# Kernel tuning notes

Measured on AMD Instinct MI355X. Metric: run time of the kernel, lower is better.

Reference implementation:

```python
import jax, jax.numpy as jnp
import numpy as np

V = 50257      # num_class
H = 512        # hid_size
EMB = 256      # embedding_size
E = 128        # emb_cond_size
COND_RANGE = (10, 20, 30)
NCSEQ = 100    # num_cond_seq_class
T, B = 64, 32
TC = 32        # cond_seq length


def _gru_scan(x, h0, Wih, Whh, bih, bhh):
    """PyTorch-convention GRU. x: [T,B,in], h0: [B,Hd]. Gate order: r,z,n."""
    Hd = h0.shape[-1]
    xw = jnp.einsum('tbi,gi->tbg', x, Wih) + bih  # [T,B,3H]

    def step(h, xw_t):
        hw = h @ Whh.T + bhh
        r = jax.nn.sigmoid(xw_t[:, :Hd] + hw[:, :Hd])
        z = jax.nn.sigmoid(xw_t[:, Hd:2 * Hd] + hw[:, Hd:2 * Hd])
        n = jnp.tanh(xw_t[:, 2 * Hd:] + r * hw[:, 2 * Hd:])
        hn = (1.0 - z) * n + z * h
        return hn, hn

    hT, outs = jax.lax.scan(step, h0, xw)
    return outs, hT


def setup_inputs() -> dict:
    key = jax.random.key(0)
    ks = jax.random.split(key, 24)
    s = 0.02
    inp = {
        'input_data': jax.random.randint(ks[0], (T, B), 0, V),
        'condition': jnp.stack([jax.random.randint(ks[1 + i], (B,), 0, COND_RANGE[i]) for i in range(3)], 0),
        'cond_seq': jax.random.randint(ks[4], (TC, B), 0, NCSEQ),
        'emb_cond_0': jax.random.normal(ks[5], (COND_RANGE[0], E)) * s,
        'emb_cond_1': jax.random.normal(ks[6], (COND_RANGE[1], E)) * s,
        'emb_cond_2': jax.random.normal(ks[7], (COND_RANGE[2], E)) * s,
        'cond_seq_emb': jax.random.normal(ks[8], (NCSEQ, E)) * s,
        'embedding': jax.random.normal(ks[9], (V, EMB)) * s,
        'attn_W': jax.random.normal(ks[10], (H, E + H)) * s,
        'attn_b': jnp.zeros((H,), jnp.float32),
        'v_W': jax.random.normal(ks[11], (1, H)) * s,
        'gru_Wih': jax.random.normal(ks[12], (3 * H, EMB)) * s,
        'gru_Whh': jax.random.normal(ks[13], (3 * H, H)) * s,
        'gru_bih': jnp.zeros((3 * H,), jnp.float32),
        'gru_bhh': jnp.zeros((3 * H,), jnp.float32),
        'cgru_Wih': jax.random.normal(ks[14], (3 * E, E)) * s,
        'cgru_Whh': jax.random.normal(ks[15], (3 * E, E)) * s,
        'cgru_bih': jnp.zeros((3 * E,), jnp.float32),
        'cgru_bhh': jnp.zeros((3 * E,), jnp.float32),
        'dense_W': jax.random.normal(ks[16], (V, E + EMB + H)) * s,
        'dense_b': jnp.zeros((V,), jnp.float32),
    }
    return inp


def reference(input_data, condition, cond_seq,
              emb_cond_0, emb_cond_1, emb_cond_2, cond_seq_emb, embedding,
              attn_W, attn_b, v_W,
              gru_Wih, gru_Whh, gru_bih, gru_bhh,
              cgru_Wih, cgru_Whh, cgru_bih, cgru_bhh,
              dense_W, dense_b):
    Tl, Bl = input_data.shape
    # conditional embeddings: [num_cond, B, E]
    tables = (emb_cond_0, emb_cond_1, emb_cond_2)
    cond_emb = jnp.stack([tables[i][condition[i]] for i in range(3)], axis=0)
    # conditional sequence GRU encoder: [TC, B, E]
    cseq_in = cond_seq_emb[cond_seq]
    cseq_out, _ = _gru_scan(cseq_in, jnp.zeros((Bl, E), cseq_in.dtype),
                            cgru_Wih, cgru_Whh, cgru_bih, cgru_bhh)
    enc = jnp.concatenate([cond_emb, cseq_out], axis=0)  # [S, B, E]
    enc_b = jnp.transpose(enc, (1, 0, 2))                # [B, S, E]

    # Bahdanau attention: split attn weight into encoder/decoder parts
    W_e = attn_W[:, :E]   # [H, E]
    W_h = attn_W[:, E:]   # [H, H]
    enc_proj = jnp.einsum('bse,he->bsh', enc_b, W_e)     # precompute once

    x_emb = embedding[input_data]                        # [T, B, EMB]
    xw = jnp.einsum('tbi,gi->tbg', x_emb, gru_Wih) + gru_bih  # [T, B, 3H]

    def step(h, inputs):
        xe_t, xw_t = inputs
        # attention against previous hidden h
        score = jnp.tanh(enc_proj + (h @ W_h.T + attn_b)[:, None, :]) @ v_W[0]  # [B,S]
        w = jax.nn.softmax(score, axis=1)
        c = jnp.einsum('bs,bse->be', w, enc_b)           # [B, E]
        # GRU cell
        hw = h @ gru_Whh.T + gru_bhh
        r = jax.nn.sigmoid(xw_t[:, :H] + hw[:, :H])
        z = jax.nn.sigmoid(xw_t[:, H:2 * H] + hw[:, H:2 * H])
        n = jnp.tanh(xw_t[:, 2 * H:] + r * hw[:, 2 * H:])
        hn = (1.0 - z) * n + z * h
        # output head uses context, input embedding and PREVIOUS hidden h
        logits = jnp.concatenate([c, xe_t, h], axis=-1) @ dense_W.T + dense_b
        pred = jax.nn.log_softmax(logits, axis=-1)
        return hn, (pred, w)

    h0 = jnp.zeros((Bl, H), x_emb.dtype)
    hT, (total_pred, weights) = jax.lax.scan(step, h0, (x_emb, xw))
    return total_pred, hT[None, :, :], weights


if __name__ == '__main__':
    out = reference(**setup_inputs())
    print([o.shape for o in out])
```

## Files before the change

### kernel.cpp

```cpp
#include <hip/hip_runtime.h>
#include <hip/hip_bf16.h>
#include <hip/hip_cooperative_groups.h>
#include <math.h>

namespace cg = cooperative_groups;

#define Tt 64
#define Bb 32
#define Hh 512
#define EMBe 256
#define Ee 128
#define Ss 35
#define Vv 50257
#define Kk 896
#define TCc 32
#define VPAD 50304
#define NTILE 393

typedef __bf16 bf16_t;
typedef __bf16 bf16x4 __attribute__((ext_vector_type(4)));
typedef __bf16 bf16x8 __attribute__((ext_vector_type(8)));
typedef float f32x4 __attribute__((ext_vector_type(4)));

#define POIS32 0x7FC07FC0u

__device__ __forceinline__ float sigf(float x){ return 1.f/(1.f + expf(-x)); }

__device__ __forceinline__ void gll16(const void* g, void* l){
  __builtin_amdgcn_global_load_lds(
      (const __attribute__((address_space(1))) unsigned int*)g,
      (__attribute__((address_space(3))) unsigned int*)l, 16, 0, 0);
}

#define DOT4(acc, W_, H_) acc += (W_).x*(H_).x + (W_).y*(H_).y + (W_).z*(H_).z + (W_).w*(H_).w

__global__ void k_cond_emb(const int* __restrict__ cond, const float* __restrict__ t0,
                           const float* __restrict__ t1, const float* __restrict__ t2,
                           float* __restrict__ enc){
  int g = blockIdx.x*blockDim.x + threadIdx.x;
  if (g >= 3*Bb*Ee) return;
  int i = g/(Bb*Ee); int b = (g/Ee)%Bb; int e = g%Ee;
  const float* tbl = (i==0)? t0 : (i==1)? t1 : t2;
  int ci = cond[i*Bb + b];
  enc[(size_t)i*Bb*Ee + b*Ee + e] = tbl[(size_t)ci*Ee + e];
}

__global__ void k_cxw(const int* __restrict__ cond_seq, const float* __restrict__ cemb,
                      const float* __restrict__ Wih, const float* __restrict__ bih,
                      float* __restrict__ cxw){
  __shared__ float es[Ee];
  int row = blockIdx.x; int tid = threadIdx.x;
  int idx = cond_seq[row];
  es[tid] = cemb[(size_t)idx*Ee + tid];
  __syncthreads();
  const float4* hp = (const float4*)es;
  for (int q = 0; q < 3; ++q){
    int g = q*Ee + tid;
    const float4* wr = (const float4*)(Wih + (size_t)g*Ee);
    float acc = bih[g];
    #pragma unroll 8
    for (int k = 0; k < Ee/4; ++k){ float4 w4 = wr[k]; float4 h4 = hp[k]; DOT4(acc, w4, h4); }
    cxw[(size_t)row*(3*Ee) + g] = acc;
  }
}

__global__ void k_xemb(const int* __restrict__ input_data, const float* __restrict__ emb,
                       bf16_t* __restrict__ xe){
  int row = blockIdx.x, tid = threadIdx.x;
  int idx = input_data[row];
  xe[(size_t)row*EMBe + tid] = (bf16_t)emb[(size_t)idx*EMBe + tid];
}

__global__ void k_ctrans(const float* __restrict__ W, float* __restrict__ WT){
  int idx = blockIdx.x*256 + threadIdx.x;
  if (idx >= 3*Ee*Ee) return;
  int g = idx/Ee, k = idx%Ee;
  WT[(size_t)k*(3*Ee) + g] = W[idx];
}

__global__ void k_cseq_scan(const float* __restrict__ cxw, const float* __restrict__ WT,
                            const float* __restrict__ bhh, float* __restrict__ enc){
  __shared__ float hs[Ee];
  int b = blockIdx.x; int j = threadIdx.x;
  hs[j] = 0.f; __syncthreads();
  float b0 = bhh[j], b1 = bhh[Ee+j], b2 = bhh[2*Ee+j];
  for (int t = 0; t < TCc; ++t){
    const float* xp = cxw + ((size_t)t*Bb + b)*(3*Ee);
    float a0=b0, a1=b1, a2=b2;
    #pragma unroll 4
    for (int k = 0; k < Ee; ++k){
      float hk = hs[k];
      const float* wr = WT + (size_t)k*(3*Ee);
      a0 += hk * wr[j];
      a1 += hk * wr[Ee + j];
      a2 += hk * wr[2*Ee + j];
    }
    float r = sigf(xp[j] + a0);
    float z = sigf(xp[Ee + j] + a1);
    float n = tanhf(xp[2*Ee + j] + r*a2);
    float hcur = hs[j];
    float hn = (1.f - z)*n + z*hcur;
    __syncthreads();
    hs[j] = hn;
    enc[(size_t)(3+t)*Bb*Ee + b*Ee + j] = hn;
    __syncthreads();
  }
}

__global__ void k_encproj(const float* __restrict__ enc, const float* __restrict__ attn_W,
                          float* __restrict__ enc_proj){
  __shared__ float es[Ee];
  int blk = blockIdx.x; int tid = threadIdx.x;
  int b = blk/Ss, s = blk%Ss;
  if (tid < Ee) es[tid] = enc[(size_t)s*Bb*Ee + b*Ee + tid];
  __syncthreads();
  const float4* hp = (const float4*)es;
  for (int q = 0; q < 2; ++q){
    int hh = q*256 + tid;
    const float4* wr = (const float4*)(attn_W + (size_t)hh*(Ee+Hh));
    float acc = 0.f;
    #pragma unroll 8
    for (int k = 0; k < Ee/4; ++k){ float4 w4 = wr[k]; float4 h4 = hp[k]; DOT4(acc, w4, h4); }
    enc_proj[(size_t)blk*Hh + hh] = acc;
  }
}

#define HSLOT (Bb*Hh)

__global__ void k_poison(bf16_t* __restrict__ hsteps){
  size_t i = (size_t)blockIdx.x*256 + threadIdx.x;
  size_t total = (size_t)(Tt+1)*HSLOT/2;
  if (i >= total) return;
  unsigned v = (i < HSLOT/2) ? 0u : POIS32;
  __hip_atomic_store((unsigned*)hsteps + i, v, __ATOMIC_RELAXED, __HIP_MEMORY_SCOPE_AGENT);
}

#define SCAN_BLOCKS_L 128
#define SCAN_WORK 16
#define SCAN_THREADS 384
#define WSL_STRIDE 520
#define HST_STRIDE 520
#define GW_STRIDE 104
#define SCAN_LDS (96*WSL_STRIDE*2 + Bb*HST_STRIDE*2 + Bb*GW_STRIDE*4)
#define NCH 11

__global__ __launch_bounds__(SCAN_THREADS) void k_scan_coop(
    const float* __restrict__ xw, const float* __restrict__ Whh,
    const float* __restrict__ bhh, float* __restrict__ h_all,
    bf16_t* __restrict__ hsteps, const float* __restrict__ Wd,
    bf16_t* __restrict__ Wb, int wbf){
  extern __shared__ char smem[];
  const int tid = threadIdx.x;
  const int blk = blockIdx.x;

  if (blk >= SCAN_WORK){
    if (wbf){
      size_t total = (size_t)VPAD*Kk/8;
      size_t stride = (size_t)(SCAN_BLOCKS_L - SCAN_WORK)*SCAN_THREADS;
      for (size_t c = (size_t)(blk - SCAN_WORK)*SCAN_THREADS + tid; c < total; c += stride){
        size_t i = c*8;
        size_t row = i / Kk;
        int col = (int)(i % Kk);
        bf16x8 o;
        if (row < Vv){
          float4 f0 = *(const float4*)(Wd + i);
          float4 f1 = *(const float4*)(Wd + i + 4);
          o[0]=(bf16_t)f0.x; o[1]=(bf16_t)f0.y; o[2]=(bf16_t)f0.z; o[3]=(bf16_t)f0.w;
          o[4]=(bf16_t)f1.x; o[5]=(bf16_t)f1.y; o[6]=(bf16_t)f1.z; o[7]=(bf16_t)f1.w;
        } else {
          #pragma unroll
          for (int k = 0; k < 8; ++k) o[k] = (bf16_t)0.f;
        }
        int kk = col >> 6, u = (col & 63) >> 3;
        int rs = (int)(row & 7);
        *(bf16x8*)(Wb + row*Kk + (kk << 6) + ((u ^ rs) << 3)) = o;
      }
    }
    return;
  }

  bf16_t* Wsl = (bf16_t*)smem;
  bf16_t* hst = (bf16_t*)(smem + 96*WSL_STRIDE*2);
  float*  gw  = (float*) (smem + 96*WSL_STRIDE*2 + Bb*HST_STRIDE*2);
  const int c0 = blk*32;

  for (int lr = 0; lr < 96; ++lr){
    int g = lr >> 5, i = lr & 31;
    const float* src = Whh + ((size_t)g*Hh + c0 + i)*Hh;
    for (int c = tid; c < Hh; c += SCAN_THREADS)
      Wsl[lr*WSL_STRIDE + c] = (bf16_t)src[c];
  }
  for (int idx = tid; idx < Bb*16; idx += SCAN_THREADS){
    int b = idx >> 4, u = idx & 15;
    float* hp = &h_all[(size_t)b*Hh + c0 + u*2];
    hp[0] = 0.f; hp[1] = 0.f;
  }

  const int npair = (tid < 128) ? 2 : 1;
  int pb[2], pc[2];
  float bh0[2][2], bh1[2][2], bh2[2][2], hreg[2][2];
  for (int p = 0; p < npair; ++p){
    int pid = tid + p*SCAN_THREADS;
    pb[p] = pid >> 4; pc[p] = (pid & 15)*2;
    for (int c = 0; c < 2; ++c){
      int j = c0 + pc[p] + c;
      bh0[p][c] = bhh[j]; bh1[p][c] = bhh[Hh + j]; bh2[p][c] = bhh[2*Hh + j];
      hreg[p][c] = 0.f;
    }
  }
  __syncthreads();

  const int wid = tid >> 6, lane = tid & 63;
  const int l15 = lane & 15, l4 = lane >> 4;

  for (int t = 0; t < Tt; ++t){
    {
      const unsigned long long* hinU = (const unsigned long long*)(hsteps + (size_t)t*HSLOT);
      unsigned long long v[NCH];
      int nmine = 0;
      #pragma unroll
      for (int k = 0; k < NCH; ++k){
        int idx = tid + k*SCAN_THREADS;
        if (idx < Bb*Hh/4){
          v[k] = __hip_atomic_load(hinU + idx, __ATOMIC_RELAXED, __HIP_MEMORY_SCOPE_AGENT);
          nmine = k + 1;
        }
      }
      #pragma unroll
      for (int k = 0; k < NCH; ++k){
        if (k < nmine){
          int idx = tid + k*SCAN_THREADS;
          while ((unsigned)v[k] == POIS32 || (unsigned)(v[k] >> 32) == POIS32){
            __builtin_amdgcn_s_sleep(1);
            v[k] = __hip_atomic_load(hinU + idx, __ATOMIC_RELAXED, __HIP_MEMORY_SCOPE_AGENT);
          }
        }
      }
      #pragma unroll
      for (int k = 0; k < NCH; ++k){
        if (k < nmine){
          int idx = tid + k*SCAN_THREADS;
          int b = idx >> 7, c4 = idx & 127;
          *((unsigned long long*)(hst + (size_t)b*HST_STRIDE) + c4) = v[k];
        }
      }
    }
    __syncthreads();

    f32x4 acc0 = {0.f,0.f,0.f,0.f}, acc1 = {0.f,0.f,0.f,0.f};
    #pragma unroll
    for (int ks = 0; ks < 16; ++ks){
      bf16x8 bfr = *(const bf16x8*)(Wsl + (wid*16 + l15)*WSL_STRIDE + ks*32 + l4*8);
      bf16x8 a0  = *(const bf16x8*)(hst + l15*HST_STRIDE        + ks*32 + l4*8);
      bf16x8 a1  = *(const bf16x8*)(hst + (16 + l15)*HST_STRIDE + ks*32 + l4*8);
      acc0 = __builtin_amdgcn_mfma_f32_16x16x32_bf16(a0, bfr, acc0, 0, 0, 0);
      acc1 = __builtin_amdgcn_mfma_f32_16x16x32_bf16(a1, bfr, acc1, 0, 0, 0);
    }
    #pragma unroll
    for (int i = 0; i < 4; ++i){
      gw[(l4*4 + i)*GW_STRIDE + wid*16 + l15]        = acc0[i];
      gw[(16 + l4*4 + i)*GW_STRIDE + wid*16 + l15]   = acc1[i];
    }
    __syncthreads();

    unsigned* houtU = (unsigned*)(hsteps + (size_t)(t+1)*HSLOT);
    for (int p = 0; p < npair; ++p){
      int b = pb[p], cl = pc[p];
      const float* xp = xw + ((size_t)t*Bb + b)*(3*Hh);
      float hn2[2];
      #pragma unroll
      for (int c = 0; c < 2; ++c){
        int j = c0 + cl + c;
        float gr = gw[b*GW_STRIDE + cl + c]      + bh0[p][c];
        float gz = gw[b*GW_STRIDE + 32 + cl + c] + bh1[p][c];
        float gn = gw[b*GW_STRIDE + 64 + cl + c] + bh2[p][c];
        float r = sigf(xp[j] + gr);
        float z = sigf(xp[Hh + j] + gz);
        float n = tanhf(xp[2*Hh + j] + r*gn);
        float hn = (1.f - z)*n + z*hreg[p][c];
        hreg[p][c] = hn; hn2[c] = hn;
      }
      unsigned u0 = (unsigned)__builtin_bit_cast(unsigned short, (bf16_t)hn2[0]);
      unsigned u1 = (unsigned)__builtin_bit_cast(unsigned short, (bf16_t)hn2[1]);
      __hip_atomic_store(houtU + ((b*Hh + c0 + cl) >> 1), u0 | (u1 << 16),
                         __ATOMIC_RELAXED, __HIP_MEMORY_SCOPE_AGENT);
    }
    for (int p = 0; p < npair; ++p){
      int b = pb[p], cl = pc[p];
      float* hp = &h_all[((size_t)(t+1)*Bb + b)*Hh + c0 + cl];
      hp[0] = hreg[p][0]; hp[1] = hreg[p][1];
    }
  }
}

#define SG_LDS (256*64*2)
#define SWZ(rowv, uv) (((size_t)(rowv))*64 + ((((uv) ^ ((rowv)&7)))<<3))

template<int KTOT, int LDB>
__global__ __launch_bounds__(256) void k_sgemm(const bf16_t* __restrict__ A,
                                               const float* __restrict__ B,
                                               const float* __restrict__ bias,
                                               float* __restrict__ C, int N){
  extern __shared__ char smem[];
  bf16_t* As = (bf16_t*)smem;
  bf16_t* Ws = As + 128*64;
  const int tid = threadIdx.x, bid = blockIdx.x;
  const int mt = bid & 15, nt = bid >> 4;
  const int m0 = mt*128, n0 = nt*128;
  const int srow = tid >> 1, sub = (tid & 1)*4;
  const int NKK2 = KTOT/64;

  int4 aR[4]; float4 wF[8];
#define SLOADA(KK) { \
    const int4* p = (const int4*)(A + (size_t)(m0 + srow)*KTOT + (KK)*64 + sub*8); \
    aR[0]=p[0]; aR[1]=p[1]; aR[2]=p[2]; aR[3]=p[3]; }
#define SLOADW(KK) { \
    const float4* p = (const float4*)(B + (size_t)(n0 + srow)*LDB + (KK)*64 + sub*8); \
    _Pragma("unroll") for (int r = 0; r < 8; ++r) wF[r] = p[r]; }
#define SSTORES() { \
    _Pragma("unroll") \
    for (int j = 0; j < 4; ++j) \
      *(int4*)(As + SWZ(srow, sub + j)) = aR[j]; \
    _Pragma("unroll") for (int j = 0; j < 4; ++j){ \
      bf16x8 p8; \
      p8[0]=(bf16_t)wF[2*j].x; p8[1]=(bf16_t)wF[2*j].y; p8[2]=(bf16_t)wF[2*j].z; p8[3]=(bf16_t)wF[2*j].w; \
      p8[4]=(bf16_t)wF[2*j+1].x; p8[5]=(bf16_t)wF[2*j+1].y; p8[6]=(bf16_t)wF[2*j+1].z; p8[7]=(bf16_t)wF[2*j+1].w; \
      *(bf16x8*)(Ws + SWZ(srow, sub + j)) = p8; \
    } }

  const int wave = tid >> 6, lane = tid & 63;
  const int l15 = lane & 15, l4 = lane >> 4;
  const int mh = (wave >> 1)*64, nh = (wave & 1)*64;

  f32x4 acc[4][4];
  #pragma unroll
  for (int i = 0; i < 4; ++i)
    #pragma unroll
    for (int j = 0; j < 4; ++j) acc[i][j] = (f32x4){0.f,0.f,0.f,0.f};

  SLOADA(0); SLOADW(0);
  SSTORES();
  __syncthreads();
  for (int kk = 0; kk < NKK2; ++kk){
    if (kk + 1 < NKK2){ SLOADA(kk + 1); SLOADW(kk + 1); }
    #pragma unroll
    for (int k32 = 0; k32 < 2; ++k32){
      const int u = k32*4 + l4;
      bf16x8 aF[4], bF[4];
      #pragma unroll
      for (int mf = 0; mf < 4; ++mf)
        aF[mf] = *(const bf16x8*)(As + SWZ(mh + mf*16 + l15, u));
      #pragma unroll
      for (int nf = 0; nf < 4; ++nf)
        bF[nf] = *(const bf16x8*)(Ws + SWZ(nh + nf*16 + l15, u));
      #pragma unroll
      for (int mf = 0; mf < 4; ++mf)
        #pragma unroll
        for (int nf = 0; nf < 4; ++nf)
          acc[mf][nf] = __builtin_amdgcn_mfma_f32_16x16x32_bf16(aF[mf], bF[nf], acc[mf][nf], 0, 0, 0);
    }
    __syncthreads();
    if (kk + 1 < NKK2){
      SSTORES();
      __syncthreads();
    }
  }
  #pragma unroll
  for (int mf = 0; mf < 4; ++mf){
    #pragma unroll
    for (int nf = 0; nf < 4; ++nf){
      int v = n0 + nh + nf*16 + l15;
      float bv = bias[v];
      int m = m0 + mh + mf*16 + l4*4;
      #pragma unroll
      for (int i = 0; i < 4; ++i)
        C[(size_t)(m + i)*N + v] = acc[mf][nf][i] + bv;
    }
  }
#undef SLOADA
#undef SLOADW
#undef SSTORES
}

__global__ void k_score(const float* __restrict__ hw_attn, const float* __restrict__ enc_proj,
                        const float* __restrict__ enc, const float* __restrict__ vW,
                        float* __restrict__ w_out, float* __restrict__ c_all){
  __shared__ float hws[Hh];
  __shared__ float sc[Ss];
  __shared__ float wsm[Ss];
  int row = blockIdx.x, lane = threadIdx.x;
  int b = row & (Bb-1);
  for (int k = lane; k < Hh; k += 64) hws[k] = hw_attn[(size_t)row*Hh + k];
  __syncthreads();
  for (int s = 0; s < Ss; ++s){
    const float* ep = enc_proj + ((size_t)b*Ss + s)*Hh;
    float acc = 0.f;
    for (int k = lane; k < Hh; k += 64) acc += tanhf(ep[k] + hws[k]) * vW[k];
    #pragma unroll
    for (int off = 32; off > 0; off >>= 1) acc += __shfl_xor(acc, off);
    if (lane == 0) sc[s] = acc;
  }
  __syncthreads();
  float val = (lane < Ss) ? sc[lane] : -3.0e38f;
  float mx = val;
  #pragma unroll
  for (int off = 32; off > 0; off >>= 1) mx = fmaxf(mx, __shfl_xor(mx, off));
  float e = (lane < Ss) ? expf(val - mx) : 0.f;
  float sm = e;
  #pragma unroll
  for (int off = 32; off > 0; off >>= 1) sm += __shfl_xor(sm, off);
  float w = e / sm;
  if (lane < Ss){ w_out[(size_t)row*Ss + lane] = w; wsm[lane] = w; }
  __syncthreads();
  for (int q = 0; q < 2; ++q){
    int ee = q*64 + lane;
    float acc = 0.f;
    #pragma unroll
    for (int s = 0; s < Ss; ++s) acc += wsm[s]*enc[(size_t)s*Bb*Ee + b*Ee + ee];
    c_all[(size_t)row*Ee + ee] = acc;
  }
}

__global__ void k_abuild(const int* __restrict__ input_data, const float* __restrict__ c_all,
                         const float* __restrict__ embedding, const float* __restrict__ h_all,
                         bf16_t* __restrict__ A){
  int row = blockIdx.x, tid = threadIdx.x;
  int xidx = input_data[row];
  bf16_t* Ar = A + (size_t)row*Kk;
  int rs = row & 7;
  for (int col = tid; col < Kk; col += 256){
    float v;
    if (col < Ee) v = c_all[(size_t)row*Ee + col];
    else if (col < Ee + EMBe) v = embedding[(size_t)xidx*EMBe + (col - Ee)];
    else v = h_all[(size_t)row*Hh + (col - Ee - EMBe)];
    int kk = col >> 6, u = (col & 63) >> 3, e = col & 7;
    Ar[(kk << 6) + ((u ^ rs) << 3) + e] = (bf16_t)v;
  }
}

#define BM 128
#define BN 128
#define BK 64
#define NKK (Kk/BK)
#define BUFSZ ((BM + BN)*BK)
#define GEMM_LDS (2*BUFSZ*2)
#define NEGINF (-1.0e30f)

__device__ __forceinline__ void lse_comb(float& m, float& s, float om, float os){
  if (om > m){ s = s*expf(m - om) + os; m = om; }
  else        s = s + os*expf(om - m);
}

template<int WBF>
__global__ __launch_bounds__(256) void k_gemm7(const bf16_t* __restrict__ A,
                                               const void* __restrict__ Wsrc,
                                               const float* __restrict__ bias,
                                               float* __restrict__ out,
                                               float2* __restrict__ partials){
  extern __shared__ char smem[];
  const int tid = threadIdx.x;
  const int bid = blockIdx.x;
  const int mt = bid & 15, nt = bid >> 4;
  const int m0 = mt*BM, n0 = nt*BN;
  const int wave = tid >> 6, lane = tid & 63;
  const int l15 = lane & 15, l4 = lane >> 4;
  const int mh = (wave >> 1)*64, nh = (wave & 1)*64;

  f32x4 acc[4][4];
  #pragma unroll
  for (int i = 0; i < 4; ++i)
    #pragma unroll
    for (int j = 0; j < 4; ++j) acc[i][j] = (f32x4){0.f,0.f,0.f,0.f};

  if (WBF){
    const char* Ag = (const char*)A;
    const char* Wg = (const char*)Wsrc;
    bf16_t* bufs = (bf16_t*)smem;
    const int grow = tid >> 3;
    const size_t gcol = (size_t)(tid & 7)*16;
    {
      char* Asb = (char*)bufs;
      char* Wsb = Asb + BM*BK*2;
      #pragma unroll
      for (int j = 0; j < 4; ++j){
        gll16(Ag + (size_t)(m0 + j*32 + grow)*(Kk*2) + gcol, Asb + j*4096 + tid*16);
        gll16(Wg + (size_t)(n0 + j*32 + grow)*(Kk*2) + gcol, Wsb + j*4096 + tid*16);
      }
    }
    int cur = 0;
    for (int kk = 0; kk < NKK; ++kk){
      __syncthreads();
      if (kk + 1 < NKK){
        size_t ko = (size_t)(kk + 1)*128;
        char* Asb = (char*)(bufs + (cur ^ 1)*BUFSZ);
        char* Wsb = Asb + BM*BK*2;
        #pragma unroll
        for (int j = 0; j < 4; ++j){
          gll16(Ag + (size_t)(m0 + j*32 + grow)*(Kk*2) + ko + gcol, Asb + j*4096 + tid*16);
          gll16(Wg + (size_t)(n0 + j*32 + grow)*(Kk*2) + ko + gcol, Wsb + j*4096 + tid*16);
        }
      }
      const bf16_t* As = bufs + cur*BUFSZ;
      const bf16_t* Ws = As + BM*BK;
      #pragma unroll
      for (int k32 = 0; k32 < 2; ++k32){
        const int u = k32*4 + l4;
        bf16x8 aF[4], bF[4];
        #pragma unroll
        for (int mf = 0; mf < 4; ++mf)
          aF[mf] = *(const bf16x8*)(As + SWZ(mh + mf*16 + l15, u));
        #pragma unroll
        for (int nf = 0; nf < 4; ++nf)
          bF[nf] = *(const bf16x8*)(Ws + SWZ(nh + nf*16 + l15, u));
        #pragma unroll
        for (int mf = 0; mf < 4; ++mf)
          #pragma unroll
          for (int nf = 0; nf < 4; ++nf)
            acc[mf][nf] = __builtin_amdgcn_mfma_f32_16x16x32_bf16(aF[mf], bF[nf], acc[mf][nf], 0, 0, 0);
      }
      cur ^= 1;
    }
  } else {
    bf16_t* As = (bf16_t*)smem;
    bf16_t* Ws = As + BM*BK;
    const int srow = tid >> 1, sub = (tid & 1)*4;
    int4 aR[4]; float4 wF[8];
    const float* Wf = (const float*)Wsrc;
#define LOADA(KK) { \
    const int4* p = (const int4*)(A + (size_t)(m0 + srow)*Kk + (KK)*BK + sub*8); \
    aR[0]=p[0]; aR[1]=p[1]; aR[2]=p[2]; aR[3]=p[3]; }
#define LOADW(KK) { \
    int vrow = n0 + srow; \
    if (vrow < Vv){ \
      const float4* p = (const float4*)(Wf + (size_t)vrow*Kk + (KK)*BK + sub*8); \
      _Pragma("unroll") for (int r = 0; r < 8; ++r) wF[r] = p[r]; \
    } else { \
      _Pragma("unroll") for (int r = 0; r < 8; ++r) wF[r] = make_float4(0.f,0.f,0.f,0.f); \
    } }
#define STORES() { \
    _Pragma("unroll") \
    for (int j = 0; j < 4; ++j) \
      *(int4*)(As + (size_t)srow*64 + (size_t)(sub + j)*8) = aR[j]; \
    _Pragma("unroll") for (int j = 0; j < 4; ++j){ \
      bf16x8 p8; \
      p8[0]=(bf16_t)wF[2*j].x; p8[1]=(bf16_t)wF[2*j].y; p8[2]=(bf16_t)wF[2*j].z; p8[3]=(bf16_t)wF[2*j].w; \
      p8[4]=(bf16_t)wF[2*j+1].x; p8[5]=(bf16_t)wF[2*j+1].y; p8[6]=(bf16_t)wF[2*j+1].z; p8[7]=(bf16_t)wF[2*j+1].w; \
      *(bf16x8*)(Ws + SWZ(srow, sub + j)) = p8; \
    } }
    LOADA(0); LOADW(0);
    STORES();
    __syncthreads();
    for (int kk = 0; kk < NKK; ++kk){
      if (kk + 1 < NKK){ LOADA(kk + 1); LOADW(kk + 1); }
      #pragma unroll
      for (int k32 = 0; k32 < 2; ++k32){
        const int u = k32*4 + l4;
        bf16x8 aF[4], bF[4];
        #pragma unroll
        for (int mf = 0; mf < 4; ++mf)
          aF[mf] = *(const bf16x8*)(As + SWZ(mh + mf*16 + l15, u));
        #pragma unroll
        for (int nf = 0; nf < 4; ++nf)
          bF[nf] = *(const bf16x8*)(Ws + SWZ(nh + nf*16 + l15, u));
        #pragma unroll
        for (int mf = 0; mf < 4; ++mf)
          #pragma unroll
          for (int nf = 0; nf < 4; ++nf)
            acc[mf][nf] = __builtin_amdgcn_mfma_f32_16x16x32_bf16(aF[mf], bF[nf], acc[mf][nf], 0, 0, 0);
      }
      __syncthreads();
      if (kk + 1 < NKK){
        STORES();
        __syncthreads();
      }
    }
#undef LOADA
#undef LOADW
#undef STORES
  }
  float bv4[4];
  #pragma unroll
  for (int nf = 0; nf < 4; ++nf){
    int v = n0 + nh + nf*16 + l15;
    bv4[nf] = (v < Vv) ? bias[v] : 0.f;
  }
  __syncthreads();
  float2* epls = (float2*)smem;
  #pragma unroll
  for (int mf = 0; mf < 4; ++mf){
    #pragma unroll
    for (int i = 0; i < 4; ++i){
      float vals[4]; float m = NEGINF;
      #pragma unroll
      for (int nf = 0; nf < 4; ++nf){
        int v = n0 + nh + nf*16 + l15;
        float x = acc[mf][nf][i] + bv4[nf];
        vals[nf] = (v < Vv) ? x : NEGINF;
        if (v < Vv){
          out[(size_t)(m0 + mh + mf*16 + l4*4 + i)*Vv + v] = x;
          if (vals[nf] > m) m = vals[nf];
        }
      }
      float s = 0.f;
      #pragma unroll
      for (int nf = 0; nf < 4; ++nf)
        if (vals[nf] > NEGINF) s += expf(vals[nf] - m);
      #pragma unroll
      for (int off = 1; off < 16; off <<= 1){
        float om = __shfl_xor(m, off);
        float os = __shfl_xor(s, off);
        lse_comb(m, s, om, os);
      }
      if (l15 == 0){
        int rl = mh + mf*16 + l4*4 + i;
        epls[rl*2 + (wave & 1)] = make_float2(m, s);
      }
    }
  }
  __syncthreads();
  if (tid < BM){
    float2 a = epls[tid*2 + 0];
    float2 b = epls[tid*2 + 1];
    float m = a.x, s = a.y;
    lse_comb(m, s, b.x, b.y);
    partials[(size_t)(m0 + tid)*512 + nt] = make_float2(m, s);
  }
}

__global__ void k_lsecomb(const float2* __restrict__ partials, float* __restrict__ lse){
  int row = blockIdx.x*4 + (threadIdx.x >> 6);
  int lane = threadIdx.x & 63;
  const float2* p = partials + (size_t)row*512;
  float m = NEGINF, s = 0.f;
  for (int nt = lane; nt < NTILE; nt += 64){
    float2 v = p[nt];
    lse_comb(m, s, v.x, v.y);
  }
  #pragma unroll
  for (int off = 32; off > 0; off >>= 1){
    float om = __shfl_xor(m, off);
    float os = __shfl_xor(s, off);
    lse_comb(m, s, om, os);
  }
  if (lane == 0) lse[row] = m + logf(s);
}

__global__ void k_sub(float* __restrict__ pred, const float* __restrict__ lse){
  int row = blockIdx.x, tid = threadIdx.x;
  float l = lse[row];
  float* p = pred + (size_t)row*Vv;
  int pre = (int)(((16 - (((size_t)p) & 15)) & 15) >> 2);
  if (tid < pre) p[tid] -= l;
  int n4 = (Vv - pre) >> 2;
  float4* p4 = (float4*)(p + pre);
  for (int v = tid; v < n4; v += 256){
    float4 x = p4[v];
    x.x -= l; x.y -= l; x.z -= l; x.w -= l;
    p4[v] = x;
  }
  int tl = pre + n4*4 + tid;
  if (tl < Vv) p[tl] -= l;
}

__global__ void k_hT(const float* __restrict__ h_all, float* __restrict__ hT){
  int g = blockIdx.x*256 + threadIdx.x;
  if (g < Bb*Hh) hT[g] = h_all[(size_t)Tt*Bb*Hh + g];
}

extern "C" void kernel_launch(void* const* d_in, const int* in_sizes, int n_in,
                              void* d_out, int out_size, void* d_ws, size_t ws_size,
                              hipStream_t stream){
  const int*   input_data = (const int*)d_in[0];
  const int*   condition  = (const int*)d_in[1];
  const int*   cond_seq   = (const int*)d_in[2];
  const float* emb_c0     = (const float*)d_in[3];
  const float* emb_c1     = (const float*)d_in[4];
  const float* emb_c2     = (const float*)d_in[5];
  const float* cseq_emb   = (const float*)d_in[6];
  const float* embedding  = (const float*)d_in[7];
  const float* attn_W     = (const float*)d_in[8];
  const float* attn_b     = (const float*)d_in[9];
  const float* v_W        = (const float*)d_in[10];
  const float* gru_Wih    = (const float*)d_in[11];
  const float* gru_Whh    = (const float*)d_in[12];
  const float* gru_bih    = (const float*)d_in[13];
  const float* gru_bhh    = (const float*)d_in[14];
  const float* cgru_Wih   = (const float*)d_in[15];
  const float* cgru_Whh   = (const float*)d_in[16];
  const float* cgru_bih   = (const float*)d_in[17];
  const float* cgru_bhh   = (const float*)d_in[18];
  const float* dense_W    = (const float*)d_in[19];
  const float* dense_b    = (const float*)d_in[20];

  float* out    = (float*)d_out;
  float* pred   = out;
  float* hT_out = out + (size_t)Tt*Bb*Vv;
  float* w_out  = hT_out + (size_t)Bb*Hh;

  float* ws       = (float*)d_ws;
  float* h_all    = ws;
  float* xw       = h_all + (size_t)(Tt+1)*Bb*Hh;
  float* cxw      = xw + (size_t)Tt*Bb*3*Hh;
  float* enc      = cxw + (size_t)TCc*Bb*3*Ee;
  float* enc_proj = enc + (size_t)Ss*Bb*Ee;
  float* hw_attn  = enc_proj + (size_t)Bb*Ss*Hh;
  float* c_all    = hw_attn + (size_t)Tt*Bb*Hh;
  float* lse      = c_all + (size_t)Tt*Bb*Ee;
  bf16_t* Abf     = (bf16_t*)(lse + Tt*Bb);
  bf16_t* hsteps  = Abf + (size_t)Tt*Bb*Kk;
  float* WTc      = (float*)(hsteps + (size_t)(Tt+1)*HSLOT);
  int*   bar      = (int*)(WTc + 128*3*Ee);
  float2* partials= (float2*)(bar + 256);
  bf16_t* xemb    = (bf16_t*)(partials + (size_t)Tt*Bb*512);
  bf16_t* Wb      = xemb + (size_t)Tt*Bb*EMBe;
  size_t need_b   = (size_t)((char*)(Wb + (size_t)VPAD*Kk) - (char*)d_ws);
  bool use_wbf    = (ws_size >= need_b);

  k_cond_emb<<<48, 256, 0, stream>>>(condition, emb_c0, emb_c1, emb_c2, enc);
  k_cxw<<<TCc*Bb, 128, 0, stream>>>(cond_seq, cseq_emb, cgru_Wih, cgru_bih, cxw);
  k_xemb<<<Tt*Bb, 256, 0, stream>>>(input_data, embedding, xemb);
  k_sgemm<EMBe, EMBe><<<16*12, 256, SG_LDS, stream>>>(xemb, gru_Wih, gru_bih, xw, 3*Hh);
  k_ctrans<<<(3*Ee*Ee + 255)/256, 256, 0, stream>>>(cgru_Whh, WTc);
  k_cseq_scan<<<Bb, Ee, 0, stream>>>(cxw, WTc, cgru_bhh, enc);
  k_encproj<<<Bb*Ss, 256, 0, stream>>>(enc, attn_W, enc_proj);
  {
    int npb = (int)(((size_t)(Tt+1)*HSLOT/2 + 255)/256);
    k_poison<<<npb, 256, 0, stream>>>(hsteps);
  }

  (void)hipFuncSetAttribute((const void*)k_scan_coop, hipFuncAttributeMaxDynamicSharedMemorySize, SCAN_LDS);
  {
    void* xw_p = (void*)xw; void* whh_p = (void*)gru_Whh; void* bhh_p = (void*)gru_bhh;
    void* ha_p = (void*)h_all; void* hs_p = (void*)hsteps;
    void* wd_p = (void*)dense_W; void* wb_p = (void*)Wb;
    int wbf = use_wbf ? 1 : 0;
    void* args[] = {&xw_p, &whh_p, &bhh_p, &ha_p, &hs_p, &wd_p, &wb_p, &wbf};
    (void)hipLaunchCooperativeKernel((const void*)k_scan_coop, dim3(SCAN_BLOCKS_L), dim3(SCAN_THREADS),
                                     args, SCAN_LDS, stream);
  }

  k_sgemm<Hh, (Ee+Hh)><<<16*4, 256, SG_LDS, stream>>>(hsteps, attn_W + Ee, attn_b, hw_attn, Hh);
  k_score<<<Tt*Bb, 64, 0, stream>>>(hw_attn, enc_proj, enc, v_W, w_out, c_all);
  k_abuild<<<Tt*Bb, 256, 0, stream>>>(input_data, c_all, embedding, h_all, Abf);

  (void)hipFuncSetAttribute((const void*)k_gemm7<1>, hipFuncAttributeMaxDynamicSharedMemorySize, GEMM_LDS);
  (void)hipFuncSetAttribute((const void*)k_gemm7<0>, hipFuncAttributeMaxDynamicSharedMemorySize, GEMM_LDS);
  if (use_wbf){
    k_gemm7<1><<<16*((Vv + BN - 1)/BN), 256, GEMM_LDS, stream>>>(Abf, (const void*)Wb, dense_b, pred, partials);
  } else {
    k_gemm7<0><<<16*((Vv + BN - 1)/BN), 256, GEMM_LDS, stream>>>(Abf, (const void*)dense_W, dense_b, pred, partials);
  }

  k_lsecomb<<<Tt*Bb/4, 256, 0, stream>>>(partials, lse);
  k_sub<<<Tt*Bb, 256, 0, stream>>>(pred, lse);
  k_hT<<<64, 256, 0, stream>>>(h_all, hT_out);
}
```

Measured before the change: 1.649 ms.

## Fold encoder projection into idle scan blocks; deepen GEMM pipeline with BK=32 ring

Removes the separate encoder-projection kernel and computes it inside the otherwise idle blocks of the cooperative scan kernel, before they convert dense weights to bf16. It also reworks the main logits GEMM to use a 4-slot ring buffer of BK=32 tiles with three tiles in flight, controlled by explicit vmcnt waits, in place of double-buffered BK=64. The swizzle layout of the bf16 weights and the A matrix changes to match. The aim is to cut one launch and hide more global-load latency in the dominant GEMM, at the cost of more barriers per K-step and a dependence on hand-written wait counts.

Result: faster. 1.601 ms (-2.9%).

```diff
diff --git a/kernel.cpp b/kernel.cpp
--- a/kernel.cpp
+++ b/kernel.cpp
@@ -107,24 +107,6 @@
   }
 }
 
-__global__ void k_encproj(const float* __restrict__ enc, const float* __restrict__ attn_W,
-                          float* __restrict__ enc_proj){
-  __shared__ float es[Ee];
-  int blk = blockIdx.x; int tid = threadIdx.x;
-  int b = blk/Ss, s = blk%Ss;
-  if (tid < Ee) es[tid] = enc[(size_t)s*Bb*Ee + b*Ee + tid];
-  __syncthreads();
-  const float4* hp = (const float4*)es;
-  for (int q = 0; q < 2; ++q){
-    int hh = q*256 + tid;
-    const float4* wr = (const float4*)(attn_W + (size_t)hh*(Ee+Hh));
-    float acc = 0.f;
-    #pragma unroll 8
-    for (int k = 0; k < Ee/4; ++k){ float4 w4 = wr[k]; float4 h4 = hp[k]; DOT4(acc, w4, h4); }
-    enc_proj[(size_t)blk*Hh + hh] = acc;
-  }
-}
-
 #define HSLOT (Bb*Hh)
 
 __global__ void k_poison(bf16_t* __restrict__ hsteps){
@@ -148,12 +130,31 @@
     const float* __restrict__ xw, const float* __restrict__ Whh,
     const float* __restrict__ bhh, float* __restrict__ h_all,
     bf16_t* __restrict__ hsteps, const float* __restrict__ Wd,
-    bf16_t* __restrict__ Wb, int wbf){
+    bf16_t* __restrict__ Wb, int wbf,
+    const float* __restrict__ enc, const float* __restrict__ attn_W,
+    float* __restrict__ enc_proj){
   extern __shared__ char smem[];
   const int tid = threadIdx.x;
   const int blk = blockIdx.x;
 
   if (blk >= SCAN_WORK){
+    {
+      float* es = (float*)smem;
+      for (int item = blk - SCAN_WORK; item < Bb*Ss; item += SCAN_BLOCKS_L - SCAN_WORK){
+        int b = item / Ss, s = item % Ss;
+        __syncthreads();
+        for (int e = tid; e < Ee; e += SCAN_THREADS) es[e] = enc[(size_t)s*Bb*Ee + b*Ee + e];
+        __syncthreads();
+        const float4* hp = (const float4*)es;
+        for (int hh = tid; hh < Hh; hh += SCAN_THREADS){
+          const float4* wr = (const float4*)(attn_W + (size_t)hh*(Ee+Hh));
+          float acc = 0.f;
+          #pragma unroll 8
+          for (int k = 0; k < Ee/4; ++k){ float4 w4 = wr[k]; float4 h4 = hp[k]; DOT4(acc, w4, h4); }
+          enc_proj[(size_t)item*Hh + hh] = acc;
+        }
+      }
+    }
     if (wbf){
       size_t total = (size_t)VPAD*Kk/8;
       size_t stride = (size_t)(SCAN_BLOCKS_L - SCAN_WORK)*SCAN_THREADS;
@@ -171,9 +172,9 @@
           #pragma unroll
           for (int k = 0; k < 8; ++k) o[k] = (bf16_t)0.f;
         }
-        int kk = col >> 6, u = (col & 63) >> 3;
-        int rs = (int)(row & 7);
-        *(bf16x8*)(Wb + row*Kk + (kk << 6) + ((u ^ rs) << 3)) = o;
+        int kk = col >> 5, u = (col & 31) >> 3;
+        int rs = (int)(row & 3);
+        *(bf16x8*)(Wb + row*Kk + (kk << 5) + ((u ^ rs) << 3)) = o;
       }
     }
     return;
@@ -427,24 +428,26 @@
   int row = blockIdx.x, tid = threadIdx.x;
   int xidx = input_data[row];
   bf16_t* Ar = A + (size_t)row*Kk;
-  int rs = row & 7;
+  int rs = row & 3;
   for (int col = tid; col < Kk; col += 256){
     float v;
     if (col < Ee) v = c_all[(size_t)row*Ee + col];
     else if (col < Ee + EMBe) v = embedding[(size_t)xidx*EMBe + (col - Ee)];
     else v = h_all[(size_t)row*Hh + (col - Ee - EMBe)];
-    int kk = col >> 6, u = (col & 63) >> 3, e = col & 7;
-    Ar[(kk << 6) + ((u ^ rs) << 3) + e] = (bf16_t)v;
+    int kk = col >> 5, u = (col & 31) >> 3, e = col & 7;
+    Ar[(kk << 5) + ((u ^ rs) << 3) + e] = (bf16_t)v;
   }
 }
 
 #define BM 128
 #define BN 128
-#define BK 64
-#define NKK (Kk/BK)
-#define BUFSZ ((BM + BN)*BK)
-#define GEMM_LDS (2*BUFSZ*2)
+#define BK2 32
+#define NKKG (Kk/BK2)
+#define TILE_B ((BM + BN)*BK2)
+#define GEMM_LDS (4*TILE_B*2)
 #define NEGINF (-1.0e30f)
+
+#define SWZ32(rowv, uv) (((size_t)(rowv))*32 + ((((uv) ^ ((rowv)&3)))<<3))
 
 __device__ __forceinline__ void lse_comb(float& m, float& s, float om, float os){
   if (om > m){ s = s*expf(m - om) + os; m = om; }
@@ -475,101 +478,88 @@
   if (WBF){
     const char* Ag = (const char*)A;
     const char* Wg = (const char*)Wsrc;
-    bf16_t* bufs = (bf16_t*)smem;
-    const int grow = tid >> 3;
-    const size_t gcol = (size_t)(tid & 7)*16;
-    {
-      char* Asb = (char*)bufs;
-      char* Wsb = Asb + BM*BK*2;
-      #pragma unroll
-      for (int j = 0; j < 4; ++j){
-        gll16(Ag + (size_t)(m0 + j*32 + grow)*(Kk*2) + gcol, Asb + j*4096 + tid*16);
-        gll16(Wg + (size_t)(n0 + j*32 + grow)*(Kk*2) + gcol, Wsb + j*4096 + tid*16);
-      }
-    }
-    int cur = 0;
-    for (int kk = 0; kk < NKK; ++kk){
-      __syncthreads();
-      if (kk + 1 < NKK){
-        size_t ko = (size_t)(kk + 1)*128;
-        char* Asb = (char*)(bufs + (cur ^ 1)*BUFSZ);
-        char* Wsb = Asb + BM*BK*2;
-        #pragma unroll
-        for (int j = 0; j < 4; ++j){
-          gll16(Ag + (size_t)(m0 + j*32 + grow)*(Kk*2) + ko + gcol, Asb + j*4096 + tid*16);
-          gll16(Wg + (size_t)(n0 + j*32 + grow)*(Kk*2) + ko + gcol, Wsb + j*4096 + tid*16);
-        }
-      }
-      const bf16_t* As = bufs + cur*BUFSZ;
-      const bf16_t* Ws = As + BM*BK;
-      #pragma unroll
-      for (int k32 = 0; k32 < 2; ++k32){
-        const int u = k32*4 + l4;
-        bf16x8 aF[4], bF[4];
-        #pragma unroll
-        for (int mf = 0; mf < 4; ++mf)
-          aF[mf] = *(const bf16x8*)(As + SWZ(mh + mf*16 + l15, u));
+    bf16_t* ring = (bf16_t*)smem;
+    const int i0 = tid, i1 = tid + 256;
+    auto issue = [&](int t){
+      char* Asb = (char*)(ring + (size_t)(t & 3)*TILE_B);
+      char* Wsb = Asb + BM*BK2*2;
+      size_t ko = (size_t)t*64;
+      gll16(Ag + (size_t)(m0 + (i0 >> 2))*(Kk*2) + ko + (size_t)(i0 & 3)*16, Asb + (size_t)i0*16);
+      gll16(Ag + (size_t)(m0 + (i1 >> 2))*(Kk*2) + ko + (size_t)(i1 & 3)*16, Asb + (size_t)i1*16);
+      gll16(Wg + (size_t)(n0 + (i0 >> 2))*(Kk*2) + ko + (size_t)(i0 & 3)*16, Wsb + (size_t)i0*16);
+      gll16(Wg + (size_t)(n0 + (i1 >> 2))*(Kk*2) + ko + (size_t)(i1 & 3)*16, Wsb + (size_t)i1*16);
+    };
+    issue(0); issue(1); issue(2);
+    for (int kk = 0; kk < NKKG; ++kk){
+      __builtin_amdgcn_sched_barrier(0);
+      if (kk + 2 < NKKG)      { asm volatile("s_waitcnt vmcnt(8)" ::: "memory"); }
+      else if (kk + 1 < NKKG) { asm volatile("s_waitcnt vmcnt(4)" ::: "memory"); }
+      else                    { asm volatile("s_waitcnt vmcnt(0)" ::: "memory"); }
+      __builtin_amdgcn_sched_barrier(0);
+      __builtin_amdgcn_s_barrier();
+      __builtin_amdgcn_sched_barrier(0);
+      if (kk + 3 < NKKG) issue(kk + 3);
+      const bf16_t* As = ring + (size_t)(kk & 3)*TILE_B;
+      const bf16_t* Ws = As + BM*BK2;
+      bf16x8 aF[4], bF[4];
+      #pragma unroll
+      for (int mf = 0; mf < 4; ++mf)
+        aF[mf] = *(const bf16x8*)(As + SWZ32(mh + mf*16 + l15, l4));
+      #pragma unroll
+      for (int nf = 0; nf < 4; ++nf)
+        bF[nf] = *(const bf16x8*)(Ws + SWZ32(nh + nf*16 + l15, l4));
+      #pragma unroll
+      for (int mf = 0; mf < 4; ++mf)
         #pragma unroll
         for (int nf = 0; nf < 4; ++nf)
-          bF[nf] = *(const bf16x8*)(Ws + SWZ(nh + nf*16 + l15, u));
-        #pragma unroll
-        for (int mf = 0; mf < 4; ++mf)
-          #pragma unroll
-          for (int nf = 0; nf < 4; ++nf)
-            acc[mf][nf] = __builtin_amdgcn_mfma_f32_16x16x32_bf16(aF[mf], bF[nf], acc[mf][nf], 0, 0, 0);
-      }
-      cur ^= 1;
+          acc[mf][nf] = __builtin_amdgcn_mfma_f32_16x16x32_bf16(aF[mf], bF[nf], acc[mf][nf], 0, 0, 0);
     }
   } else {
     bf16_t* As = (bf16_t*)smem;
-    bf16_t* Ws = As + BM*BK;
-    const int srow = tid >> 1, sub = (tid & 1)*4;
-    int4 aR[4]; float4 wF[8];
+    bf16_t* Ws = As + BM*BK2;
+    const int srow = tid >> 1, uh = (tid & 1)*2;
+    int4 aR[2]; float4 wF[4];
     const float* Wf = (const float*)Wsrc;
 #define LOADA(KK) { \
-    const int4* p = (const int4*)(A + (size_t)(m0 + srow)*Kk + (KK)*BK + sub*8); \
-    aR[0]=p[0]; aR[1]=p[1]; aR[2]=p[2]; aR[3]=p[3]; }
+    const int4* p = (const int4*)(A + (size_t)(m0 + srow)*Kk + (KK)*BK2 + uh*8); \
+    aR[0]=p[0]; aR[1]=p[1]; }
 #define LOADW(KK) { \
     int vrow = n0 + srow; \
     if (vrow < Vv){ \
-      const float4* p = (const float4*)(Wf + (size_t)vrow*Kk + (KK)*BK + sub*8); \
-      _Pragma("unroll") for (int r = 0; r < 8; ++r) wF[r] = p[r]; \
+      const float4* p = (const float4*)(Wf + (size_t)vrow*Kk + (KK)*BK2 + uh*8); \
+      _Pragma("unroll") for (int r = 0; r < 4; ++r) wF[r] = p[r]; \
     } else { \
-      _Pragma("unroll") for (int r = 0; r < 8; ++r) wF[r] = make_float4(0.f,0.f,0.f,0.f); \
+      _Pragma("unroll") for (int r = 0; r < 4; ++r) wF[r] = make_float4(0.f,0.f,0.f,0.f); \
     } }
 #define STORES() { \
     _Pragma("unroll") \
-    for (int j = 0; j < 4; ++j) \
-      *(int4*)(As + (size_t)srow*64 + (size_t)(sub + j)*8) = aR[j]; \
-    _Pragma("unroll") for (int j = 0; j < 4; ++j){ \
+    for (int j = 0; j < 2; ++j) \
+      *(int4*)(As + (size_t)srow*32 + (size_t)(uh + j)*8) = aR[j]; \
+    _Pragma("unroll") for (int j = 0; j < 2; ++j){ \
       bf16x8 p8; \
       p8[0]=(bf16_t)wF[2*j].x; p8[1]=(bf16_t)wF[2*j].y; p8[2]=(bf16_t)wF[2*j].z; p8[3]=(bf16_t)wF[2*j].w; \
       p8[4]=(bf16_t)wF[2*j+1].x; p8[5]=(bf16_t)wF[2*j+1].y; p8[6]=(bf16_t)wF[2*j+1].z; p8[7]=(bf16_t)wF[2*j+1].w; \
-      *(bf16x8*)(Ws + SWZ(srow, sub + j)) = p8; \
+      *(bf16x8*)(Ws + SWZ32(srow, uh + j)) = p8; \
     } }
     LOADA(0); LOADW(0);
     STORES();
     __syncthreads();
-    for (int kk = 0; kk < NKK; ++kk){
-      if (kk + 1 < NKK){ LOADA(kk + 1); LOADW(kk + 1); }
-      #pragma unroll
-      for (int k32 = 0; k32 < 2; ++k32){
-        const int u = k32*4 + l4;
-        bf16x8 aF[4], bF[4];
-        #pragma unroll
-        for (int mf = 0; mf < 4; ++mf)
-          aF[mf] = *(const bf16x8*)(As + SWZ(mh + mf*16 + l15, u));
+    for (int kk = 0; kk < NKKG; ++kk){
+      if (kk + 1 < NKKG){ LOADA(kk + 1); LOADW(kk + 1); }
+      bf16x8 aF[4], bF[4];
+      #pragma unroll
+      for (int mf = 0; mf < 4; ++mf)
+        aF[mf] = *(const bf16x8*)(As + SWZ32(mh + mf*16 + l15, l4));
+      #pragma unroll
+      for (int nf = 0; nf < 4; ++nf)
+        bF[nf] = *(const bf16x8*)(Ws + SWZ32(nh + nf*16 + l15, l4));
+      #pragma unroll
+      for (int mf = 0; mf < 4; ++mf)
         #pragma unroll
         for (int nf = 0; nf < 4; ++nf)
-          bF[nf] = *(const bf16x8*)(Ws + SWZ(nh + nf*16 + l15, u));
-        #pragma unroll
-        for (int mf = 0; mf < 4; ++mf)
-          #pragma unroll
-          for (int nf = 0; nf < 4; ++nf)
-            acc[mf][nf] = __builtin_amdgcn_mfma_f32_16x16x32_bf16(aF[mf], bF[nf], acc[mf][nf], 0, 0, 0);
-      }
+          acc[mf][nf] = __builtin_amdgcn_mfma_f32_16x16x32_bf16(aF[mf], bF[nf], acc[mf][nf], 0, 0, 0);
       __syncthreads();
-      if (kk + 1 < NKK){
+      if (kk + 1 < NKKG){
         STORES();
         __syncthreads();
       }
@@ -722,7 +712,6 @@
   k_sgemm<EMBe, EMBe><<<16*12, 256, SG_LDS, stream>>>(xemb, gru_Wih, gru_bih, xw, 3*Hh);
   k_ctrans<<<(3*Ee*Ee + 255)/256, 256, 0, stream>>>(cgru_Whh, WTc);
   k_cseq_scan<<<Bb, Ee, 0, stream>>>(cxw, WTc, cgru_bhh, enc);
-  k_encproj<<<Bb*Ss, 256, 0, stream>>>(enc, attn_W, enc_proj);
   {
     int npb = (int)(((size_t)(Tt+1)*HSLOT/2 + 255)/256);
     k_poison<<<npb, 256, 0, stream>>>(hsteps);
@@ -734,7 +723,9 @@
     void* ha_p = (void*)h_all; void* hs_p = (void*)hsteps;
     void* wd_p = (void*)dense_W; void* wb_p = (void*)Wb;
     int wbf = use_wbf ? 1 : 0;
-    void* args[] = {&xw_p, &whh_p, &bhh_p, &ha_p, &hs_p, &wd_p, &wb_p, &wbf};
+    void* enc_p = (void*)enc; void* aw_p = (void*)attn_W; void* ep_p = (void*)enc_proj;
+    void* args[] = {&xw_p, &whh_p, &bhh_p, &ha_p, &hs_p, &wd_p, &wb_p, &wbf,
+                    &enc_p, &aw_p, &ep_p};
     (void)hipLaunchCooperativeKernel((const void*)k_scan_coop, dim3(SCAN_BLOCKS_L), dim3(SCAN_THREADS),
                                      args, SCAN_LDS, stream);
   }
```
